# Kernel tuning notes

Hardware: AMD Instinct MI355X
Metric: run time of the kernel (lower is better)

The kernel has to match this reference:

```python
import jax, jax.numpy as jnp
import numpy as np

VOCAB = 50257

def setup_inputs() -> dict:
    key = jax.random.key(0)
    k1, k2, k3, k4 = jax.random.split(key, 4)
    B, T, S = 4, 4096, 8192  # batch, target_len, seq_len
    tokens = jax.random.randint(k1, (B, T), 0, VOCAB, dtype=jnp.int64)
    batch_input_ids = jax.random.randint(k2, (2, B, S), 0, VOCAB, dtype=jnp.int64)
    candidate_tokens = jax.random.randint(k3, (B, T), 0, VOCAB, dtype=jnp.int64)
    candidate_scores = jax.random.normal(k4, (B, T), dtype=jnp.float32)
    unmask_count = 4096
    return {"tokens": tokens, "batch_input_ids": batch_input_ids,
            "candidate_tokens": candidate_tokens, "candidate_scores": candidate_scores,
            "unmask_count": unmask_count}

def reference(tokens, batch_input_ids, candidate_tokens, candidate_scores, unmask_count):
    flat_scores = candidate_scores.reshape(-1)            # [N]
    flat_cand = candidate_tokens.reshape(-1)              # [N]
    flat_tok = tokens.reshape(-1)                         # [N]
    N = flat_scores.shape[0]
    idx = jnp.arange(N)
    # Stable 'better-than' matrix: strictly higher score, or equal score with lower index.
    better = (flat_scores[None, :] > flat_scores[:, None]) | (
        (flat_scores[None, :] == flat_scores[:, None]) & (idx[None, :] < idx[:, None]))
    rank = jnp.sum(better, axis=1)                        # [N] int
    selected = rank < jnp.asarray(unmask_count, dtype=rank.dtype)
    updated_flat = jnp.where(selected, flat_cand, flat_tok)
    updated_tokens = updated_flat.reshape(tokens.shape).astype(jnp.int64)
    S = batch_input_ids.shape[-1]
    T = tokens.shape[-1]
    upd = batch_input_ids
    upd = upd.at[0:1, :, S - T:S].set(updated_tokens[None])
    upd = upd.at[1:2, :, 0:T].set(updated_tokens[None])
    return updated_tokens, upd.astype(jnp.int64)
```

## Files before the change

### kernel.cpp

```cpp
#include <hip/hip_runtime.h>

#define NTOK 16384
#define BQ 4
#define TQ 4096
#define SQ 8192
#define BLK 1024
#define NBLK 16

__device__ __forceinline__ unsigned score_key(float s) {
    unsigned u = __float_as_uint(s);
    if ((u << 1) == 0u) u = 0u;
    return (u & 0x80000000u) ? ~u : (u | 0x80000000u);
}

__global__ __launch_bounds__(BLK) void token_update_kernel(
    const float* __restrict__ scores,
    const int* __restrict__ cand,
    const int* __restrict__ tok,
    const int* __restrict__ bids,
    const int* __restrict__ kptr,
    int* __restrict__ out0,
    int* __restrict__ out1)
{
    __shared__ int h0[2048 * 8];
    __shared__ int h1[2048];
    __shared__ int wtot[16], wsuf[16];
    __shared__ unsigned long long s_pref;
    __shared__ int s_krem, s_E;

    const int tid  = threadIdx.x;
    const int B    = blockIdx.x;
    const int lane = tid & 63;
    const int w    = tid >> 6;

    if (tid < 512) {
        int g   = B * 512 + tid;
        int o4  = g << 2;
        int c   = o4 >> 12;
        int b   = c & 3, plane = c >> 2;
        int off = o4 & 4095;
        int addr = plane ? (BQ * SQ + b * SQ + TQ + off) : (b * SQ + off);
        *(int4*)(out1 + addr) = *(const int4*)(bids + addr);
    }

    const int K = kptr[0];
    const bool none = (K <= 0), all = (K >= NTOK);
    const bool run  = !none && !all;

    #pragma unroll
    for (int r = 0; r < 4; ++r)
        *(int4*)&h0[(r * BLK + tid) * 4] = make_int4(0, 0, 0, 0);
    if (tid == 0) { s_pref = 0ull; s_krem = 1; s_E = 1; }
    __syncthreads();

    unsigned key[16];
    const float4* s4 = (const float4*)scores;
    #pragma unroll
    for (int c = 0; c < 4; ++c) {
        float4 f = s4[c * BLK + tid];
        key[c * 4 + 0] = score_key(f.x);
        key[c * 4 + 1] = score_key(f.y);
        key[c * 4 + 2] = score_key(f.z);
        key[c * 4 + 3] = score_key(f.w);
    }

    unsigned long long pref = 0ull;
    int rb = 35;

    if (run) {
        const int slot = tid & 7;
        #pragma unroll
        for (int j = 0; j < 16; ++j)
            atomicAdd(&h0[(key[j] >> 21) * 8 + slot], 1);
        __syncthreads();

        const int SH[5]   = {35, 24, 13, 2, 0};
        const int BITS[5] = {11, 11, 11, 11, 2};
        int krem = K, E = 0;

        for (int L = 0; L < 5; ++L) {
            const int sh = SH[L], bits = BITS[L];
            int c0, c1;
            if (L == 0) {
                int4 a0 = *(int4*)&h0[tid * 16];
                int4 a1 = *(int4*)&h0[tid * 16 + 4];
                int4 b0 = *(int4*)&h0[tid * 16 + 8];
                int4 b1 = *(int4*)&h0[tid * 16 + 12];
                c0 = a0.x + a0.y + a0.z + a0.w + a1.x + a1.y + a1.z + a1.w;
                c1 = b0.x + b0.y + b0.z + b0.w + b1.x + b1.y + b1.z + b1.w;
            } else {
                c0 = h1[2 * tid]; c1 = h1[2 * tid + 1];
            }
            int pairSum = c0 + c1, incl = pairSum;
            #pragma unroll
            for (int off = 1; off < 64; off <<= 1) {
                int o = __shfl_down(incl, off, 64);
                if (lane + off < 64) incl += o;
            }
            if (lane == 0) wtot[w] = incl;
            __syncthreads();
            if (tid < 16) {
                int v = wtot[tid], i2 = v;
                #pragma unroll
                for (int off = 1; off < 16; off <<= 1) {
                    int o = __shfl_down(i2, off, 64);
                    if (tid + off < 16) i2 += o;
                }
                wsuf[tid] = i2 - v;
            }
            __syncthreads();
            int sufPair = (incl - pairSum) + wsuf[w];
            int suf1 = sufPair,  n1 = suf1 + c1;
            int suf0 = n1,       n0 = suf0 + c0;
            if (n1 >= krem && suf1 < krem) {
                s_pref = (pref << bits) | (unsigned)(2 * tid + 1);
                s_krem = krem - suf1; s_E = c1;
            }
            if (n0 >= krem && suf0 < krem) {
                s_pref = (pref << bits) | (unsigned)(2 * tid);
                s_krem = krem - suf0; s_E = c0;
            }
            __syncthreads();
            pref = s_pref; krem = s_krem; E = s_E; rb = sh;
            if (krem == E || L == 4) break;

            h1[2 * tid] = 0; h1[2 * tid + 1] = 0;
            __syncthreads();
            const int nsh = SH[L + 1], nbits = BITS[L + 1];
            #pragma unroll
            for (int j = 0; j < 16; ++j) {
                int i = (((j >> 2) * BLK + tid) << 2) | (j & 3);
                unsigned long long P = ((unsigned long long)key[j] << 14)
                                     | (unsigned)(NTOK - 1 - i);
                if ((P >> (nsh + nbits)) == pref)
                    atomicAdd(&h1[(int)((P >> nsh) & ((1 << nbits) - 1))], 1);
            }
            __syncthreads();
        }
    }

    const unsigned long long Tstar =
        none ? ~0ull : (all ? 0ull : (pref << rb));

    if (tid < 256) {
        int i4 = B * 256 + tid;
        int i  = i4 << 2;
        float4 f = s4[i4];
        int4 c4 = ((const int4*)cand)[i4];
        int4 t4 = ((const int4*)tok)[i4];
        unsigned long long P0 = ((unsigned long long)score_key(f.x) << 14) | (unsigned)(NTOK - 1 - (i + 0));
        unsigned long long P1 = ((unsigned long long)score_key(f.y) << 14) | (unsigned)(NTOK - 1 - (i + 1));
        unsigned long long P2 = ((unsigned long long)score_key(f.z) << 14) | (unsigned)(NTOK - 1 - (i + 2));
        unsigned long long P3 = ((unsigned long long)score_key(f.w) << 14) | (unsigned)(NTOK - 1 - (i + 3));
        int4 v;
        v.x = (P0 >= Tstar) ? c4.x : t4.x;
        v.y = (P1 >= Tstar) ? c4.y : t4.y;
        v.z = (P2 >= Tstar) ? c4.z : t4.z;
        v.w = (P3 >= Tstar) ? c4.w : t4.w;
        ((int4*)out0)[i4] = v;
        int b = i >> 12, tt = i & 4095;
        *(int4*)(out1 + b * SQ + (SQ - TQ) + tt) = v;
        *(int4*)(out1 + BQ * SQ + b * SQ + tt) = v;
    }
}

extern "C" void kernel_launch(void* const* d_in, const int* in_sizes, int n_in,
                              void* d_out, int out_size, void* d_ws, size_t ws_size,
                              hipStream_t stream) {
    const int*   tok    = (const int*)d_in[0];
    const int*   bids   = (const int*)d_in[1];
    const int*   cand   = (const int*)d_in[2];
    const float* scores = (const float*)d_in[3];
    const int*   kptr   = (const int*)d_in[4];

    int* out0 = (int*)d_out;
    int* out1 = out0 + NTOK;

    token_update_kernel<<<NBLK, BLK, 0, stream>>>(
        scores, cand, tok, bids, kptr, out0, out1);
}
```

Before: 65.81 us.

## Restructure radix-select: 8-bit first pass with per-lane histogram, ping-pong refinement

Reworks the radix select for the top-K threshold. The first pass now uses an 8-bit digit with a 64-way lane-privatized shared histogram, which cuts atomic contention, and a single-wavefront scan over 256 bins. The refinement passes follow as 11/11/11/5-bit digits into double-buffered histograms, so zeroing the next buffer merges into the scan and a barrier is saved. Global loads of scores, candidates and tokens are also issued up front to hide latency. The trade-offs are more shared memory and higher register pressure.

```diff
diff --git a/kernel.cpp b/kernel.cpp
--- a/kernel.cpp
+++ b/kernel.cpp
@@ -6,6 +6,8 @@
 #define SQ 8192
 #define BLK 1024
 #define NBLK 16
+
+typedef unsigned long long u64;
 
 __device__ __forceinline__ unsigned score_key(float s) {
     unsigned u = __float_as_uint(s);
@@ -22,10 +24,11 @@
     int* __restrict__ out0,
     int* __restrict__ out1)
 {
-    __shared__ int h0[2048 * 8];
-    __shared__ int h1[2048];
+    __shared__ int h0[256 * 64];
+    __shared__ int hp[2][2048];
+    __shared__ int cnt[256];
     __shared__ int wtot[16], wsuf[16];
-    __shared__ unsigned long long s_pref;
+    __shared__ u64 s_pref;
     __shared__ int s_krem, s_E;
 
     const int tid  = threadIdx.x;
@@ -33,6 +36,17 @@
     const int lane = tid & 63;
     const int w    = tid >> 6;
 
+    const float4* s4 = (const float4*)scores;
+    float4 f[4];
+    #pragma unroll
+    for (int c = 0; c < 4; ++c) f[c] = s4[c * BLK + tid];
+
+    float4 ef; int4 ec, et;
+    if (tid < 256) {
+        ef = s4[B * 256 + tid];
+        ec = ((const int4*)cand)[B * 256 + tid];
+        et = ((const int4*)tok)[B * 256 + tid];
+    }
     if (tid < 512) {
         int g   = B * 512 + tid;
         int o4  = g << 2;
@@ -42,7 +56,6 @@
         int addr = plane ? (BQ * SQ + b * SQ + TQ + off) : (b * SQ + off);
         *(int4*)(out1 + addr) = *(const int4*)(bids + addr);
     }
-
     const int K = kptr[0];
     const bool none = (K <= 0), all = (K >= NTOK);
     const bool run  = !none && !all;
@@ -50,113 +63,145 @@
     #pragma unroll
     for (int r = 0; r < 4; ++r)
         *(int4*)&h0[(r * BLK + tid) * 4] = make_int4(0, 0, 0, 0);
+    *(int4*)&(((int*)hp)[tid * 4]) = make_int4(0, 0, 0, 0);
     if (tid == 0) { s_pref = 0ull; s_krem = 1; s_E = 1; }
     __syncthreads();
 
     unsigned key[16];
-    const float4* s4 = (const float4*)scores;
     #pragma unroll
     for (int c = 0; c < 4; ++c) {
-        float4 f = s4[c * BLK + tid];
-        key[c * 4 + 0] = score_key(f.x);
-        key[c * 4 + 1] = score_key(f.y);
-        key[c * 4 + 2] = score_key(f.z);
-        key[c * 4 + 3] = score_key(f.w);
-    }
-
-    unsigned long long pref = 0ull;
-    int rb = 35;
+        key[c * 4 + 0] = score_key(f[c].x);
+        key[c * 4 + 1] = score_key(f[c].y);
+        key[c * 4 + 2] = score_key(f[c].z);
+        key[c * 4 + 3] = score_key(f[c].w);
+    }
+    #pragma unroll
+    for (int j = 0; j < 16; ++j)
+        atomicAdd(&h0[(key[j] >> 24) * 64 + lane], 1);
+    __syncthreads();
+
+    {
+        int bin = tid >> 2, q = tid & 3;
+        int base = bin * 64 + q * 16;
+        int sum = 0;
+        #pragma unroll
+        for (int m = 0; m < 16; ++m)
+            sum += h0[base + ((m + bin) & 15)];
+        sum += __shfl_xor(sum, 1, 64);
+        sum += __shfl_xor(sum, 2, 64);
+        if (q == 0) cnt[bin] = sum;
+    }
+    __syncthreads();
+
+    u64 pref = 0ull;
+    int rb = 38;
 
     if (run) {
-        const int slot = tid & 7;
-        #pragma unroll
-        for (int j = 0; j < 16; ++j)
-            atomicAdd(&h0[(key[j] >> 21) * 8 + slot], 1);
-        __syncthreads();
-
-        const int SH[5]   = {35, 24, 13, 2, 0};
-        const int BITS[5] = {11, 11, 11, 11, 2};
-        int krem = K, E = 0;
-
-        for (int L = 0; L < 5; ++L) {
-            const int sh = SH[L], bits = BITS[L];
-            int c0, c1;
-            if (L == 0) {
-                int4 a0 = *(int4*)&h0[tid * 16];
-                int4 a1 = *(int4*)&h0[tid * 16 + 4];
-                int4 b0 = *(int4*)&h0[tid * 16 + 8];
-                int4 b1 = *(int4*)&h0[tid * 16 + 12];
-                c0 = a0.x + a0.y + a0.z + a0.w + a1.x + a1.y + a1.z + a1.w;
-                c1 = b0.x + b0.y + b0.z + b0.w + b1.x + b1.y + b1.z + b1.w;
-            } else {
-                c0 = h1[2 * tid]; c1 = h1[2 * tid + 1];
-            }
-            int pairSum = c0 + c1, incl = pairSum;
+        if (tid < 64) {
+            int4 c = *(int4*)&cnt[tid * 4];
+            int T = c.x + c.y + c.z + c.w;
+            int incl = T;
             #pragma unroll
             for (int off = 1; off < 64; off <<= 1) {
                 int o = __shfl_down(incl, off, 64);
-                if (lane + off < 64) incl += o;
+                if (tid + off < 64) incl += o;
             }
-            if (lane == 0) wtot[w] = incl;
-            __syncthreads();
-            if (tid < 16) {
-                int v = wtot[tid], i2 = v;
-                #pragma unroll
-                for (int off = 1; off < 16; off <<= 1) {
-                    int o = __shfl_down(i2, off, 64);
-                    if (tid + off < 16) i2 += o;
-                }
-                wsuf[tid] = i2 - v;
-            }
-            __syncthreads();
-            int sufPair = (incl - pairSum) + wsuf[w];
-            int suf1 = sufPair,  n1 = suf1 + c1;
-            int suf0 = n1,       n0 = suf0 + c0;
-            if (n1 >= krem && suf1 < krem) {
-                s_pref = (pref << bits) | (unsigned)(2 * tid + 1);
-                s_krem = krem - suf1; s_E = c1;
-            }
-            if (n0 >= krem && suf0 < krem) {
-                s_pref = (pref << bits) | (unsigned)(2 * tid);
-                s_krem = krem - suf0; s_E = c0;
-            }
-            __syncthreads();
-            pref = s_pref; krem = s_krem; E = s_E; rb = sh;
-            if (krem == E || L == 4) break;
-
-            h1[2 * tid] = 0; h1[2 * tid + 1] = 0;
-            __syncthreads();
-            const int nsh = SH[L + 1], nbits = BITS[L + 1];
+            int s3 = incl - T,  n3 = s3 + c.w;
+            int s2 = n3,        n2 = s2 + c.z;
+            int s1 = n2,        n1 = s1 + c.y;
+            int s0 = n1,        n0 = s0 + c.x;
+            if (n3 >= K && s3 < K) { s_pref = (u64)(4 * tid + 3); s_krem = K - s3; s_E = c.w; }
+            if (n2 >= K && s2 < K) { s_pref = (u64)(4 * tid + 2); s_krem = K - s2; s_E = c.z; }
+            if (n1 >= K && s1 < K) { s_pref = (u64)(4 * tid + 1); s_krem = K - s1; s_E = c.y; }
+            if (n0 >= K && s0 < K) { s_pref = (u64)(4 * tid + 0); s_krem = K - s0; s_E = c.x; }
+        }
+        __syncthreads();
+        pref = s_pref;
+        int krem = s_krem, E = s_E;
+
+        const int SH[4] = {27, 16, 5, 0};
+        for (int L = 0; L < 4 && krem != E; ++L) {
+            const int sh = SH[L];
+            const int bits = (L == 3) ? 5 : 11;
+            int* hc = hp[L & 1];
+            int* ho = hp[(L + 1) & 1];
             #pragma unroll
             for (int j = 0; j < 16; ++j) {
                 int i = (((j >> 2) * BLK + tid) << 2) | (j & 3);
-                unsigned long long P = ((unsigned long long)key[j] << 14)
-                                     | (unsigned)(NTOK - 1 - i);
-                if ((P >> (nsh + nbits)) == pref)
-                    atomicAdd(&h1[(int)((P >> nsh) & ((1 << nbits) - 1))], 1);
+                u64 P = ((u64)key[j] << 14) | (unsigned)(NTOK - 1 - i);
+                if ((P >> (sh + bits)) == pref)
+                    atomicAdd(&hc[(int)((P >> sh) & ((1 << bits) - 1))], 1);
             }
             __syncthreads();
+
+            if (bits == 11) {
+                int c0 = hc[2 * tid], c1 = hc[2 * tid + 1];
+                ho[2 * tid] = 0; ho[2 * tid + 1] = 0;
+                int pairSum = c0 + c1, incl = pairSum;
+                #pragma unroll
+                for (int off = 1; off < 64; off <<= 1) {
+                    int o = __shfl_down(incl, off, 64);
+                    if (lane + off < 64) incl += o;
+                }
+                if (lane == 0) wtot[w] = incl;
+                __syncthreads();
+                if (tid < 16) {
+                    int v = wtot[tid], i2 = v;
+                    #pragma unroll
+                    for (int off = 1; off < 16; off <<= 1) {
+                        int o = __shfl_down(i2, off, 64);
+                        if (tid + off < 16) i2 += o;
+                    }
+                    wsuf[tid] = i2 - v;
+                }
+                __syncthreads();
+                int sufPair = (incl - pairSum) + wsuf[w];
+                int suf1 = sufPair, n1 = suf1 + c1;
+                int suf0 = n1,      n0 = suf0 + c0;
+                if (n1 >= krem && suf1 < krem) {
+                    s_pref = (pref << 11) | (unsigned)(2 * tid + 1);
+                    s_krem = krem - suf1; s_E = c1;
+                }
+                if (n0 >= krem && suf0 < krem) {
+                    s_pref = (pref << 11) | (unsigned)(2 * tid);
+                    s_krem = krem - suf0; s_E = c0;
+                }
+                __syncthreads();
+            } else {
+                if (tid < 64) {
+                    int c = (tid < 32) ? hc[tid] : 0;
+                    int incl = c;
+                    #pragma unroll
+                    for (int off = 1; off < 64; off <<= 1) {
+                        int o = __shfl_down(incl, off, 64);
+                        if (tid + off < 64) incl += o;
+                    }
+                    int suf = incl - c;
+                    if (tid < 32 && incl >= krem && suf < krem) {
+                        s_pref = (pref << 5) | (unsigned)tid;
+                        s_krem = krem - suf; s_E = c;
+                    }
+                }
+                __syncthreads();
+            }
+            pref = s_pref; krem = s_krem; E = s_E; rb = sh;
         }
     }
 
-    const unsigned long long Tstar =
-        none ? ~0ull : (all ? 0ull : (pref << rb));
+    const u64 Tstar = none ? ~0ull : (all ? 0ull : (pref << rb));
 
     if (tid < 256) {
         int i4 = B * 256 + tid;
         int i  = i4 << 2;
-        float4 f = s4[i4];
-        int4 c4 = ((const int4*)cand)[i4];
-        int4 t4 = ((const int4*)tok)[i4];
-        unsigned long long P0 = ((unsigned long long)score_key(f.x) << 14) | (unsigned)(NTOK - 1 - (i + 0));
-        unsigned long long P1 = ((unsigned long long)score_key(f.y) << 14) | (unsigned)(NTOK - 1 - (i + 1));
-        unsigned long long P2 = ((unsigned long long)score_key(f.z) << 14) | (unsigned)(NTOK - 1 - (i + 2));
-        unsigned long long P3 = ((unsigned long long)score_key(f.w) << 14) | (unsigned)(NTOK - 1 - (i + 3));
+        u64 P0 = ((u64)score_key(ef.x) << 14) | (unsigned)(NTOK - 1 - (i + 0));
+        u64 P1 = ((u64)score_key(ef.y) << 14) | (unsigned)(NTOK - 1 - (i + 1));
+        u64 P2 = ((u64)score_key(ef.z) << 14) | (unsigned)(NTOK - 1 - (i + 2));
+        u64 P3 = ((u64)score_key(ef.w) << 14) | (unsigned)(NTOK - 1 - (i + 3));
         int4 v;
-        v.x = (P0 >= Tstar) ? c4.x : t4.x;
-        v.y = (P1 >= Tstar) ? c4.y : t4.y;
-        v.z = (P2 >= Tstar) ? c4.z : t4.z;
-        v.w = (P3 >= Tstar) ? c4.w : t4.w;
+        v.x = (P0 >= Tstar) ? ec.x : et.x;
+        v.y = (P1 >= Tstar) ? ec.y : et.y;
+        v.z = (P2 >= Tstar) ? ec.z : et.z;
+        v.w = (P3 >= Tstar) ? ec.w : et.w;
         ((int4*)out0)[i4] = v;
         int b = i >> 12, tt = i & 4095;
         *(int4*)(out1 + b * SQ + (SQ - TQ) + tt) = v;
```

New measurement: 67.57 us. 2.7% more time.
